# Kernel optimization log

Hardware: AMD Instinct MI355X
Metric: run time of the kernel (lower is better)

The kernel has to match this reference:

```python
import jax, jax.numpy as jnp
import numpy as np

MAX_SEQLEN = 2048  # static max sequence length (flash varlen APIs take this as a host arg)


def setup_inputs() -> dict:
    key = jax.random.key(0)
    k1, k2, k3 = jax.random.split(key, 3)
    T, H, D = 8192, 8, 128
    B = 4
    q = jax.random.normal(k1, (T, H, D), dtype=jnp.float32)
    k = jax.random.normal(k2, (T, H, D), dtype=jnp.float32)
    v = jax.random.normal(k3, (T, H, D), dtype=jnp.float32)
    cu = (jnp.arange(B + 1, dtype=jnp.int32) * (T // B))  # [0,2048,4096,6144,8192]
    return {"q": q, "k": k, "v": v, "cu_seqlens_q": cu, "cu_seqlens_k": cu}


def reference(q, k, v, cu_seqlens_q, cu_seqlens_k):
    """Varlen (ragged) multi-head attention, non-causal (flash_attn varlen default).

    q,k,v: [T, H, D] packed over sequences; cu_seqlens: [B+1] boundaries.
    Gathers each sequence into a padded [B, S, H, D] layout, computes
    per-sequence softmax(q k^T / sqrt(D)) v with padding masked, then
    scatters back to packed [T, H, D].
    """
    T, H, D = q.shape
    B = cu_seqlens_q.shape[0] - 1
    S = MAX_SEQLEN
    scale = 1.0 / jnp.sqrt(jnp.asarray(D, q.dtype))

    pos = jnp.arange(S)
    q_start = cu_seqlens_q[:-1]
    k_start = cu_seqlens_k[:-1]
    q_len = jnp.diff(cu_seqlens_q)  # [B]
    k_len = jnp.diff(cu_seqlens_k)

    q_idx = jnp.clip(q_start[:, None] + pos[None, :], 0, T - 1)  # [B, S]
    k_idx = jnp.clip(k_start[:, None] + pos[None, :], 0, T - 1)
    q_valid = pos[None, :] < q_len[:, None]  # [B, S]
    k_valid = pos[None, :] < k_len[:, None]

    qb = q[q_idx]  # [B, S, H, D]
    kb = k[k_idx]
    vb = v[k_idx]

    scores = jnp.einsum('bqhd,bkhd->bhqk', qb, kb) * scale  # [B, H, S, S]
    neg = jnp.asarray(-1e30, scores.dtype)
    scores = jnp.where(k_valid[:, None, None, :], scores, neg)
    attn = jax.nn.softmax(scores, axis=-1)
    ob = jnp.einsum('bhqk,bkhd->bqhd', attn, vb)  # [B, S, H, D]

    # zero padded query rows, then scatter-add back to packed layout
    ob = jnp.where(q_valid[:, :, None, None], ob, 0.0)
    out = jnp.zeros_like(q).at[q_idx.reshape(-1)].add(ob.reshape(B * S, H, D))
    return out
```

## Files before the change

kernel.cpp:

```cpp
#include <hip/hip_runtime.h>
#include <hip/hip_bf16.h>
#include <stdint.h>

#define HH 8
#define DD 128
#define MAXSEQ 2048
#define QBLK 128
#define KVB 64

typedef float f32x16 __attribute__((ext_vector_type(16)));
typedef short s16x8 __attribute__((ext_vector_type(8)));
typedef uint32_t u32x4v __attribute__((ext_vector_type(4)));

__device__ __forceinline__ unsigned short f2bf(float x) {
  union { float f; uint32_t u; } v; v.f = x;
  uint32_t u = v.u;
  return (unsigned short)((u + 0x7FFFu + ((u >> 16) & 1u)) >> 16);
}

__device__ __forceinline__ void gload_lds16(const unsigned short* g, unsigned short* l) {
  __builtin_amdgcn_global_load_lds((const __attribute__((address_space(1))) void*)g,
                                   (__attribute__((address_space(3))) void*)l, 16, 0, 0);
}

__global__ void kconv(const float* __restrict__ k, unsigned short* __restrict__ kb, int T) {
  long i = (long)blockIdx.x * blockDim.x + threadIdx.x;
  long total = (long)T * HH * DD / 4;
  if (i >= total) return;
  long e = i * 4;
  int d = (int)(e % DD);
  int h = (int)((e / DD) % HH);
  long t = e / (DD * HH);
  float4 a = *(const float4*)(k + e);
  ushort4 o;
  o.x = f2bf(a.x); o.y = f2bf(a.y); o.z = f2bf(a.z); o.w = f2bf(a.w);
  *(ushort4*)(kb + ((size_t)h * T + (size_t)t) * DD + d) = o;
}

__global__ void vtrans(const float* __restrict__ v, unsigned short* __restrict__ vt, int T) {
  __shared__ float tile[64][65];
  const int t0 = blockIdx.x * 64;
  const int d0 = blockIdx.y * 64;
  const int h = blockIdx.z;
  const int tid = threadIdx.x;
  const int row = tid >> 2;
  const int c0 = (tid & 3) * 16;
  const int tr = min(t0 + row, T - 1);
  const float* src = v + ((size_t)tr * HH + h) * DD + d0 + c0;
#pragma unroll
  for (int cc = 0; cc < 16; cc += 4) {
    float4 x = *(const float4*)(src + cc);
    tile[row][c0 + cc + 0] = x.x;
    tile[row][c0 + cc + 1] = x.y;
    tile[row][c0 + cc + 2] = x.z;
    tile[row][c0 + cc + 3] = x.w;
  }
  __syncthreads();
  unsigned short* dst = vt + ((size_t)h * DD + d0 + row) * (size_t)T + t0 + c0;
#pragma unroll
  for (int cc = 0; cc < 16; cc += 4) {
    if (t0 + c0 + cc + 3 < T) {
      ushort4 o;
      o.x = f2bf(tile[c0 + cc + 0][row]);
      o.y = f2bf(tile[c0 + cc + 1][row]);
      o.z = f2bf(tile[c0 + cc + 2][row]);
      o.w = f2bf(tile[c0 + cc + 3][row]);
      *(ushort4*)(dst + cc) = o;
    }
  }
}

__global__ __launch_bounds__(256, 2)
void attn_main(const float* __restrict__ q,
               const unsigned short* __restrict__ kb,
               const unsigned short* __restrict__ vt,
               const int* __restrict__ cuq,
               const int* __restrict__ cuk,
               float* __restrict__ out,
               int T, int BH) {
  extern __shared__ __align__(16) unsigned short smem[];

  const int bid = blockIdx.x;
  const int bh = bid % BH;
  const int qt = bid / BH;
  const int b = bh / HH, h = bh % HH;
  const int qs = cuq[b], qe = cuq[b + 1];
  const int ks = cuk[b], ke = cuk[b + 1];
  const int nq = min(qe - qs, MAXSEQ);
  const int nk = min(ke - ks, MAXSEQ);
  if (qt * QBLK >= nq || nk <= 0) return;

  const int tid = threadIdx.x;
  const int wave = tid >> 6;
  const int lane = tid & 63;
  const int lo = lane & 31;
  const int hi = lane >> 5;
  const int wbase8 = (tid & ~63) * 8;

  const unsigned short* kbh = kb + (size_t)h * T * DD;
  const unsigned short* vth = vt + (size_t)h * DD * (size_t)T;

  const float SC = (1.0f / 11.313708498984761f) * 1.4426950408889634f;
  const int qrow = qt * QBLK + wave * 32 + lo;
  const int qg = qs + min(qrow, nq - 1);
  const float* qp = q + ((size_t)qg * HH + h) * DD;
  s16x8 qf[8];
#pragma unroll
  for (int s = 0; s < 8; ++s) {
    const float* p0 = qp + s * 16 + hi * 8;
    float4 a = *(const float4*)(p0);
    float4 c = *(const float4*)(p0 + 4);
    union { unsigned short us[8]; s16x8 v; } u;
    u.us[0] = f2bf(a.x * SC); u.us[1] = f2bf(a.y * SC);
    u.us[2] = f2bf(a.z * SC); u.us[3] = f2bf(a.w * SC);
    u.us[4] = f2bf(c.x * SC); u.us[5] = f2bf(c.y * SC);
    u.us[6] = f2bf(c.z * SC); u.us[7] = f2bf(c.w * SC);
    qf[s] = u.v;
  }

  f32x16 Oa[4];
#pragma unroll
  for (int i = 0; i < 4; ++i)
#pragma unroll
    for (int r = 0; r < 16; ++r) Oa[i][r] = 0.0f;

  float m_run = -__builtin_inff();
  float l_run = 0.0f;

  const int nkt = (nk + KVB - 1) / KVB;

  auto stage = [&](int buf, int kt) {
    const int k0 = ks + kt * KVB;
    unsigned short* Kb = smem + buf * 8192;
    unsigned short* Vb = smem + 16384 + buf * 8192;
#pragma unroll
    for (int r = 0; r < 4; ++r) {
      const int g = r * 256 + tid;
      const int key = g >> 4, seg = g & 15;
      const int col = (seg * 8) ^ ((key & 7) << 3);
      const int gk = min(k0 + key, T - 1);
      gload_lds16(kbh + (size_t)gk * DD + col, Kb + (size_t)(r * 256) * 8 + wbase8);
    }
#pragma unroll
    for (int r = 0; r < 4; ++r) {
      const int g = r * 256 + tid;
      const int dr = g >> 3, sg = g & 7;
      const int colk = (sg * 8) ^ ((dr & 7) << 3);
      const int tc = min(k0 + colk, T - 8);
      gload_lds16(vth + (size_t)dr * T + tc, Vb + (size_t)(r * 256) * 8 + wbase8);
    }
  };

  stage(0, 0);
  __syncthreads();

  int cur = 0;
  for (int kt = 0; kt < nkt; ++kt) {
    if (kt + 1 < nkt) stage(cur ^ 1, kt + 1);

    const unsigned short* Kb = smem + cur * 8192;
    const unsigned short* Vb = smem + 16384 + cur * 8192;

    f32x16 st0, st1;
#pragma unroll
    for (int r = 0; r < 16; ++r) { st0[r] = 0.0f; st1[r] = 0.0f; }
    __builtin_amdgcn_s_setprio(1);
#pragma unroll
    for (int s = 0; s < 8; ++s) {
      {
        const int key = lo;
        const int idx = (key * DD + s * 16 + hi * 8) ^ ((key & 7) << 3);
        s16x8 kf = *(const s16x8*)(&Kb[idx]);
        st0 = __builtin_amdgcn_mfma_f32_32x32x16_bf16(kf, qf[s], st0, 0, 0, 0);
      }
      {
        const int key = 32 + lo;
        const int idx = (key * DD + s * 16 + hi * 8) ^ ((key & 7) << 3);
        s16x8 kf = *(const s16x8*)(&Kb[idx]);
        st1 = __builtin_amdgcn_mfma_f32_32x32x16_bf16(kf, qf[s], st1, 0, 0, 0);
      }
    }
    __builtin_amdgcn_s_setprio(0);

    if (kt * KVB + KVB > nk) {
#pragma unroll
      for (int r = 0; r < 16; ++r) {
        const int base = (r & 3) + 8 * (r >> 2) + 4 * hi;
        if (kt * KVB + base >= nk) st0[r] = -__builtin_inff();
        if (kt * KVB + 32 + base >= nk) st1[r] = -__builtin_inff();
      }
    }

    float tmax = -__builtin_inff();
#pragma unroll
    for (int r = 0; r < 16; ++r) tmax = fmaxf(tmax, fmaxf(st0[r], st1[r]));
    tmax = fmaxf(tmax, __shfl_xor(tmax, 32));

    if (!__all(tmax <= m_run + 8.0f)) {
      const float m_new = fmaxf(m_run, tmax);
      const float alpha = __builtin_amdgcn_exp2f(m_run - m_new);
      l_run *= alpha;
      m_run = m_new;
#pragma unroll
      for (int r = 0; r < 16; ++r) {
        const int src = (r & 3) + 8 * (r >> 2) + 4 * hi;
        const float af = __shfl(alpha, src);
        Oa[0][r] *= af; Oa[1][r] *= af; Oa[2][r] *= af; Oa[3][r] *= af;
      }
    }

    float p[32];
    float psum = 0.0f;
#pragma unroll
    for (int r = 0; r < 16; ++r) {
      p[r] = __builtin_amdgcn_exp2f(st0[r] - m_run);
      p[16 + r] = __builtin_amdgcn_exp2f(st1[r] - m_run);
      psum += p[r] + p[16 + r];
    }
    psum += __shfl_xor(psum, 32);
    l_run += psum;

    uint32_t ownu[16];
#pragma unroll
    for (int c = 0; c < 8; ++c) {
      const int t = c >> 2, rb = 4 * (c & 3);
      uint32_t w0, w1;
      asm("v_cvt_pk_bf16_f32 %0, %1, %2" : "=v"(w0) : "v"(p[t * 16 + rb + 0]), "v"(p[t * 16 + rb + 1]));
      asm("v_cvt_pk_bf16_f32 %0, %1, %2" : "=v"(w1) : "v"(p[t * 16 + rb + 2]), "v"(p[t * 16 + rb + 3]));
      ownu[c * 2 + 0] = w0;
      ownu[c * 2 + 1] = w1;
    }

    __builtin_amdgcn_s_setprio(1);
#pragma unroll
    for (int ks2 = 0; ks2 < 4; ++ks2) {
      uint32_t a0 = ownu[4 * ks2 + 0], b0 = ownu[4 * ks2 + 2];
      uint32_t a1 = ownu[4 * ks2 + 1], b1 = ownu[4 * ks2 + 3];
      asm("v_permlane32_swap_b32 %0, %1" : "+v"(a0), "+v"(b0));
      asm("v_permlane32_swap_b32 %0, %1" : "+v"(a1), "+v"(b1));
      union { uint32_t u[4]; s16x8 v; } pu;
      pu.u[0] = a0; pu.u[1] = a1; pu.u[2] = b0; pu.u[3] = b1;
#pragma unroll
      for (int dt = 0; dt < 4; ++dt) {
        const int d = dt * 32 + lo;
        const int idx = (d * KVB + ks2 * 16 + hi * 8) ^ ((d & 7) << 3);
        s16x8 vf = *(const s16x8*)(&Vb[idx]);
        Oa[dt] = __builtin_amdgcn_mfma_f32_32x32x16_bf16(pu.v, vf, Oa[dt], 0, 0, 0);
      }
    }
    __builtin_amdgcn_s_setprio(0);

    if (kt + 1 < nkt) {
      __syncthreads();
      cur ^= 1;
    }
  }

  const float linv = 1.0f / l_run;
#pragma unroll
  for (int r = 0; r < 16; ++r) {
    const int src = (r & 3) + 8 * (r >> 2) + 4 * hi;
    const float li = __shfl(linv, src);
    const int qirow = qt * QBLK + wave * 32 + src;
    if (qirow < nq) {
      float* op = out + ((size_t)(qs + qirow) * HH + h) * DD;
      op[0 * 32 + lo] = Oa[0][r] * li;
      op[1 * 32 + lo] = Oa[1][r] * li;
      op[2 * 32 + lo] = Oa[2][r] * li;
      op[3 * 32 + lo] = Oa[3][r] * li;
    }
  }
}

extern "C" void kernel_launch(void* const* d_in, const int* in_sizes, int n_in,
                              void* d_out, int out_size, void* d_ws, size_t ws_size,
                              hipStream_t stream) {
  const float* q = (const float*)d_in[0];
  const float* k = (const float*)d_in[1];
  const float* v = (const float*)d_in[2];
  const int* cuq = (const int*)d_in[3];
  const int* cuk = (const int*)d_in[4];
  float* out = (float*)d_out;
  const int T = in_sizes[0] / (HH * DD);
  const int B = in_sizes[3] - 1;

  hipMemsetAsync(d_out, 0, (size_t)out_size * sizeof(float), stream);

  unsigned short* kb = (unsigned short*)d_ws;
  unsigned short* vt = kb + (size_t)T * HH * DD;
  const size_t need = (size_t)T * HH * DD * 2 * 2;
  if (ws_size < need) return;

  {
    long total4 = (long)T * HH * DD / 4;
    int blocks = (int)((total4 + 255) / 256);
    kconv<<<blocks, 256, 0, stream>>>(k, kb, T);
  }
  {
    dim3 g((unsigned)((T + 63) / 64), DD / 64, HH);
    vtrans<<<g, 256, 0, stream>>>(v, vt, T);
  }
  {
    const int BH = B * HH;
    const int scap = MAXSEQ < T ? MAXSEQ : T;
    const int qtiles = (scap + QBLK - 1) / QBLK;
    attn_main<<<BH * qtiles, 256, 65536, stream>>>(q, kb, vt, cuq, cuk, out, T, BH);
  }
}
```

Measured before the change: 115.5 us.

## Split KV range across two wave groups per block and merge softmax partials

The attention block grows to 512 threads, with two groups of four waves each processing half of the key range (up to 1024 keys each) over 32-key tiles. At the end the two partial softmax states are merged through shared memory. The V tile layout in LDS is reworked for the smaller tile. The full-output memset is replaced by a kernel that zeroes only rows not covered by any sequence. The intent is more waves per CU to hide latency and less memset traffic, at the cost of smaller MFMA tiles per sync, more barriers, and a merge epilogue.

```diff
diff --git a/kernel.cpp b/kernel.cpp
--- a/kernel.cpp
+++ b/kernel.cpp
@@ -6,11 +6,10 @@
 #define DD 128
 #define MAXSEQ 2048
 #define QBLK 128
-#define KVB 64
+#define KVB 32
 
 typedef float f32x16 __attribute__((ext_vector_type(16)));
 typedef short s16x8 __attribute__((ext_vector_type(8)));
-typedef uint32_t u32x4v __attribute__((ext_vector_type(4)));
 
 __device__ __forceinline__ unsigned short f2bf(float x) {
   union { float f; uint32_t u; } v; v.f = x;
@@ -21,6 +20,22 @@
 __device__ __forceinline__ void gload_lds16(const unsigned short* g, unsigned short* l) {
   __builtin_amdgcn_global_load_lds((const __attribute__((address_space(1))) void*)g,
                                    (__attribute__((address_space(3))) void*)l, 16, 0, 0);
+}
+
+__global__ void zero_rows(const int* __restrict__ cuq, float* __restrict__ out, int T, int B) {
+  const int t = blockIdx.x * blockDim.x + threadIdx.x;
+  if (t >= T) return;
+  bool covered = false;
+  for (int b = 0; b < B; ++b) {
+    const int s = cuq[b];
+    const int len = min(cuq[b + 1] - s, MAXSEQ);
+    if (t >= s && t < s + len) covered = true;
+  }
+  if (!covered) {
+    float4* p = (float4*)(out + (size_t)t * HH * DD);
+#pragma unroll 4
+    for (int i = 0; i < HH * DD / 4; ++i) p[i] = float4{0.f, 0.f, 0.f, 0.f};
+  }
 }
 
 __global__ void kconv(const float* __restrict__ k, unsigned short* __restrict__ kb, int T) {
@@ -70,7 +85,7 @@
   }
 }
 
-__global__ __launch_bounds__(256, 2)
+__global__ __launch_bounds__(512, 4)
 void attn_main(const float* __restrict__ q,
                const unsigned short* __restrict__ kb,
                const unsigned short* __restrict__ vt,
@@ -95,13 +110,14 @@
   const int lane = tid & 63;
   const int lo = lane & 31;
   const int hi = lane >> 5;
-  const int wbase8 = (tid & ~63) * 8;
+  const int wq = wave & 3;
+  const int wk = wave >> 2;
 
   const unsigned short* kbh = kb + (size_t)h * T * DD;
   const unsigned short* vth = vt + (size_t)h * DD * (size_t)T;
 
   const float SC = (1.0f / 11.313708498984761f) * 1.4426950408889634f;
-  const int qrow = qt * QBLK + wave * 32 + lo;
+  const int qrow = qt * QBLK + wq * 32 + lo;
   const int qg = qs + min(qrow, nq - 1);
   const float* qp = q + ((size_t)qg * HH + h) * DD;
   s16x8 qf[8];
@@ -127,27 +143,28 @@
   float m_run = -__builtin_inff();
   float l_run = 0.0f;
 
-  const int nkt = (nk + KVB - 1) / KVB;
+  const int len_wk = min(nk - wk * 1024, 1024);
+  const int myT = len_wk > 0 ? (len_wk + KVB - 1) / KVB : 0;
+  const int nkt = (min(nk, 1024) + KVB - 1) / KVB;
 
   auto stage = [&](int buf, int kt) {
-    const int k0 = ks + kt * KVB;
-    unsigned short* Kb = smem + buf * 8192;
-    unsigned short* Vb = smem + 16384 + buf * 8192;
-#pragma unroll
-    for (int r = 0; r < 4; ++r) {
-      const int g = r * 256 + tid;
-      const int key = g >> 4, seg = g & 15;
-      const int col = (seg * 8) ^ ((key & 7) << 3);
-      const int gk = min(k0 + key, T - 1);
-      gload_lds16(kbh + (size_t)gk * DD + col, Kb + (size_t)(r * 256) * 8 + wbase8);
-    }
-#pragma unroll
-    for (int r = 0; r < 4; ++r) {
-      const int g = r * 256 + tid;
-      const int dr = g >> 3, sg = g & 7;
-      const int colk = (sg * 8) ^ ((dr & 7) << 3);
-      const int tc = min(k0 + colk, T - 8);
-      gload_lds16(vth + (size_t)dr * T + tc, Vb + (size_t)(r * 256) * 8 + wbase8);
+#pragma unroll
+    for (int wkk = 0; wkk < 2; ++wkk) {
+      unsigned short* slot = smem + (size_t)(wkk * 2 + buf) * 8192;
+      const int kb0 = ks + wkk * 1024 + kt * KVB;
+      {
+        const int key = tid >> 4, seg = tid & 15;
+        const int col = (seg * 8) ^ ((key & 7) << 3);
+        const int gk = min(kb0 + key, T - 1);
+        gload_lds16(kbh + (size_t)gk * DD + col, slot + (size_t)(tid & ~63) * 8);
+      }
+      {
+        const int r = tid >> 3, ph = tid & 7;
+        const int tt = ph ^ (r & 7);
+        const int d = 2 * r + (tt >> 2);
+        const int tc = min(kb0 + (tt & 3) * 8, T - 8);
+        gload_lds16(vth + (size_t)d * T + tc, slot + 4096 + (size_t)(tid & ~63) * 8);
+      }
     }
   };
 
@@ -158,97 +175,89 @@
   for (int kt = 0; kt < nkt; ++kt) {
     if (kt + 1 < nkt) stage(cur ^ 1, kt + 1);
 
-    const unsigned short* Kb = smem + cur * 8192;
-    const unsigned short* Vb = smem + 16384 + cur * 8192;
-
-    f32x16 st0, st1;
-#pragma unroll
-    for (int r = 0; r < 16; ++r) { st0[r] = 0.0f; st1[r] = 0.0f; }
-    __builtin_amdgcn_s_setprio(1);
-#pragma unroll
-    for (int s = 0; s < 8; ++s) {
-      {
-        const int key = lo;
-        const int idx = (key * DD + s * 16 + hi * 8) ^ ((key & 7) << 3);
-        s16x8 kf = *(const s16x8*)(&Kb[idx]);
-        st0 = __builtin_amdgcn_mfma_f32_32x32x16_bf16(kf, qf[s], st0, 0, 0, 0);
-      }
-      {
-        const int key = 32 + lo;
-        const int idx = (key * DD + s * 16 + hi * 8) ^ ((key & 7) << 3);
-        s16x8 kf = *(const s16x8*)(&Kb[idx]);
-        st1 = __builtin_amdgcn_mfma_f32_32x32x16_bf16(kf, qf[s], st1, 0, 0, 0);
-      }
-    }
-    __builtin_amdgcn_s_setprio(0);
-
-    if (kt * KVB + KVB > nk) {
+    if (kt < myT) {
+      const unsigned short* Kl = smem + (size_t)(wk * 2 + cur) * 8192;
+      const unsigned short* Vl = Kl + 4096;
+
+      f32x16 st;
+#pragma unroll
+      for (int r = 0; r < 16; ++r) st[r] = 0.0f;
+      __builtin_amdgcn_s_setprio(1);
+#pragma unroll
+      for (int s = 0; s < 8; ++s) {
+        const int idx = (lo * DD + s * 16 + hi * 8) ^ ((lo & 7) << 3);
+        s16x8 kf = *(const s16x8*)(&Kl[idx]);
+        st = __builtin_amdgcn_mfma_f32_32x32x16_bf16(kf, qf[s], st, 0, 0, 0);
+      }
+      __builtin_amdgcn_s_setprio(0);
+
+      const int lim = len_wk - kt * KVB;
+      if (lim < KVB) {
+#pragma unroll
+        for (int r = 0; r < 16; ++r) {
+          const int base = (r & 3) + 8 * (r >> 2) + 4 * hi;
+          if (base >= lim) st[r] = -__builtin_inff();
+        }
+      }
+
+      float tmax = -__builtin_inff();
+#pragma unroll
+      for (int r = 0; r < 16; ++r) tmax = fmaxf(tmax, st[r]);
+      tmax = fmaxf(tmax, __shfl_xor(tmax, 32));
+
+      if (!__all(tmax <= m_run + 8.0f)) {
+        const float m_new = fmaxf(m_run, tmax);
+        const float alpha = __builtin_amdgcn_exp2f(m_run - m_new);
+        l_run *= alpha;
+        m_run = m_new;
+#pragma unroll
+        for (int r = 0; r < 16; ++r) {
+          const int src = (r & 3) + 8 * (r >> 2) + 4 * hi;
+          const float af = __shfl(alpha, src);
+          Oa[0][r] *= af; Oa[1][r] *= af; Oa[2][r] *= af; Oa[3][r] *= af;
+        }
+      }
+
+      float p[16];
+      float psum = 0.0f;
 #pragma unroll
       for (int r = 0; r < 16; ++r) {
-        const int base = (r & 3) + 8 * (r >> 2) + 4 * hi;
-        if (kt * KVB + base >= nk) st0[r] = -__builtin_inff();
-        if (kt * KVB + 32 + base >= nk) st1[r] = -__builtin_inff();
-      }
-    }
-
-    float tmax = -__builtin_inff();
-#pragma unroll
-    for (int r = 0; r < 16; ++r) tmax = fmaxf(tmax, fmaxf(st0[r], st1[r]));
-    tmax = fmaxf(tmax, __shfl_xor(tmax, 32));
-
-    if (!__all(tmax <= m_run + 8.0f)) {
-      const float m_new = fmaxf(m_run, tmax);
-      const float alpha = __builtin_amdgcn_exp2f(m_run - m_new);
-      l_run *= alpha;
-      m_run = m_new;
-#pragma unroll
-      for (int r = 0; r < 16; ++r) {
-        const int src = (r & 3) + 8 * (r >> 2) + 4 * hi;
-        const float af = __shfl(alpha, src);
-        Oa[0][r] *= af; Oa[1][r] *= af; Oa[2][r] *= af; Oa[3][r] *= af;
-      }
-    }
-
-    float p[32];
-    float psum = 0.0f;
-#pragma unroll
-    for (int r = 0; r < 16; ++r) {
-      p[r] = __builtin_amdgcn_exp2f(st0[r] - m_run);
-      p[16 + r] = __builtin_amdgcn_exp2f(st1[r] - m_run);
-      psum += p[r] + p[16 + r];
-    }
-    psum += __shfl_xor(psum, 32);
-    l_run += psum;
-
-    uint32_t ownu[16];
-#pragma unroll
-    for (int c = 0; c < 8; ++c) {
-      const int t = c >> 2, rb = 4 * (c & 3);
-      uint32_t w0, w1;
-      asm("v_cvt_pk_bf16_f32 %0, %1, %2" : "=v"(w0) : "v"(p[t * 16 + rb + 0]), "v"(p[t * 16 + rb + 1]));
-      asm("v_cvt_pk_bf16_f32 %0, %1, %2" : "=v"(w1) : "v"(p[t * 16 + rb + 2]), "v"(p[t * 16 + rb + 3]));
-      ownu[c * 2 + 0] = w0;
-      ownu[c * 2 + 1] = w1;
-    }
-
-    __builtin_amdgcn_s_setprio(1);
-#pragma unroll
-    for (int ks2 = 0; ks2 < 4; ++ks2) {
-      uint32_t a0 = ownu[4 * ks2 + 0], b0 = ownu[4 * ks2 + 2];
-      uint32_t a1 = ownu[4 * ks2 + 1], b1 = ownu[4 * ks2 + 3];
-      asm("v_permlane32_swap_b32 %0, %1" : "+v"(a0), "+v"(b0));
-      asm("v_permlane32_swap_b32 %0, %1" : "+v"(a1), "+v"(b1));
-      union { uint32_t u[4]; s16x8 v; } pu;
-      pu.u[0] = a0; pu.u[1] = a1; pu.u[2] = b0; pu.u[3] = b1;
-#pragma unroll
-      for (int dt = 0; dt < 4; ++dt) {
-        const int d = dt * 32 + lo;
-        const int idx = (d * KVB + ks2 * 16 + hi * 8) ^ ((d & 7) << 3);
-        s16x8 vf = *(const s16x8*)(&Vb[idx]);
-        Oa[dt] = __builtin_amdgcn_mfma_f32_32x32x16_bf16(pu.v, vf, Oa[dt], 0, 0, 0);
-      }
-    }
-    __builtin_amdgcn_s_setprio(0);
+        p[r] = __builtin_amdgcn_exp2f(st[r] - m_run);
+        psum += p[r];
+      }
+      psum += __shfl_xor(psum, 32);
+      l_run += psum;
+
+      uint32_t ownu[8];
+#pragma unroll
+      for (int c = 0; c < 4; ++c) {
+        uint32_t w0, w1;
+        asm("v_cvt_pk_bf16_f32 %0, %1, %2" : "=v"(w0) : "v"(p[4 * c + 0]), "v"(p[4 * c + 1]));
+        asm("v_cvt_pk_bf16_f32 %0, %1, %2" : "=v"(w1) : "v"(p[4 * c + 2]), "v"(p[4 * c + 3]));
+        ownu[c * 2 + 0] = w0;
+        ownu[c * 2 + 1] = w1;
+      }
+
+      __builtin_amdgcn_s_setprio(1);
+#pragma unroll
+      for (int ks2 = 0; ks2 < 2; ++ks2) {
+        uint32_t a0 = ownu[4 * ks2 + 0], b0 = ownu[4 * ks2 + 2];
+        uint32_t a1 = ownu[4 * ks2 + 1], b1 = ownu[4 * ks2 + 3];
+        asm("v_permlane32_swap_b32 %0, %1" : "+v"(a0), "+v"(b0));
+        asm("v_permlane32_swap_b32 %0, %1" : "+v"(a1), "+v"(b1));
+        union { uint32_t u[4]; s16x8 v; } pu;
+        pu.u[0] = a0; pu.u[1] = a1; pu.u[2] = b0; pu.u[3] = b1;
+#pragma unroll
+        for (int dt = 0; dt < 4; ++dt) {
+          const int r = dt * 16 + (lo >> 1);
+          const int ph = ((lo & 1) * 4 + ks2 * 2 + hi) ^ ((lo >> 1) & 7);
+          const int idx = r * 64 + ph * 8;
+          s16x8 vf = *(const s16x8*)(&Vl[idx]);
+          Oa[dt] = __builtin_amdgcn_mfma_f32_32x32x16_bf16(pu.v, vf, Oa[dt], 0, 0, 0);
+        }
+      }
+      __builtin_amdgcn_s_setprio(0);
+    }
 
     if (kt + 1 < nkt) {
       __syncthreads();
@@ -256,18 +265,51 @@
     }
   }
 
-  const float linv = 1.0f / l_run;
-#pragma unroll
-  for (int r = 0; r < 16; ++r) {
-    const int src = (r & 3) + 8 * (r >> 2) + 4 * hi;
-    const float li = __shfl(linv, src);
-    const int qirow = qt * QBLK + wave * 32 + src;
-    if (qirow < nq) {
-      float* op = out + ((size_t)(qs + qirow) * HH + h) * DD;
-      op[0 * 32 + lo] = Oa[0][r] * li;
-      op[1 * 32 + lo] = Oa[1][r] * li;
-      op[2 * 32 + lo] = Oa[2][r] * li;
-      op[3 * 32 + lo] = Oa[3][r] * li;
+  float* fsm = (float*)smem;
+  __syncthreads();
+  if (hi == 0) {
+    fsm[wk * 256 + wq * 64 + lo] = m_run;
+    fsm[wk * 256 + wq * 64 + 32 + lo] = l_run;
+  }
+  __syncthreads();
+  const int po = (wk ^ 1) * 256 + wq * 64 + lo;
+  const float m_o = fsm[po];
+  const float l_o = fsm[po + 32];
+  const float mstar = fmaxf(m_run, m_o);
+  const float a_own = (l_run == 0.f) ? 0.f : __builtin_amdgcn_exp2f(m_run - mstar);
+  const float a_oth = (l_o == 0.f) ? 0.f : __builtin_amdgcn_exp2f(m_o - mstar);
+  __syncthreads();
+
+  if (wk == 1) {
+#pragma unroll
+    for (int r = 0; r < 16; ++r) {
+      const int src = (r & 3) + 8 * (r >> 2) + 4 * hi;
+      const float af = __shfl(a_own, src);
+      float* row = fsm + (size_t)wq * 4096 + (size_t)src * 128;
+      row[0 * 32 + lo] = Oa[0][r] * af;
+      row[1 * 32 + lo] = Oa[1][r] * af;
+      row[2 * 32 + lo] = Oa[2][r] * af;
+      row[3 * 32 + lo] = Oa[3][r] * af;
+    }
+  }
+  __syncthreads();
+  if (wk == 0) {
+    const float lst = a_own * l_run + a_oth * l_o;
+    const float linv = 1.0f / lst;
+#pragma unroll
+    for (int r = 0; r < 16; ++r) {
+      const int src = (r & 3) + 8 * (r >> 2) + 4 * hi;
+      const float af = __shfl(a_own, src);
+      const float li = __shfl(linv, src);
+      const int qirow = qt * QBLK + wq * 32 + src;
+      if (qirow < nq) {
+        const float* row = fsm + (size_t)wq * 4096 + (size_t)src * 128;
+        float* op = out + ((size_t)(qs + qirow) * HH + h) * DD;
+        op[0 * 32 + lo] = (Oa[0][r] * af + row[0 * 32 + lo]) * li;
+        op[1 * 32 + lo] = (Oa[1][r] * af + row[1 * 32 + lo]) * li;
+        op[2 * 32 + lo] = (Oa[2][r] * af + row[2 * 32 + lo]) * li;
+        op[3 * 32 + lo] = (Oa[3][r] * af + row[3 * 32 + lo]) * li;
+      }
     }
   }
 }
@@ -284,14 +326,15 @@
   const int T = in_sizes[0] / (HH * DD);
   const int B = in_sizes[3] - 1;
 
-  hipMemsetAsync(d_out, 0, (size_t)out_size * sizeof(float), stream);
-
   unsigned short* kb = (unsigned short*)d_ws;
   unsigned short* vt = kb + (size_t)T * HH * DD;
   const size_t need = (size_t)T * HH * DD * 2 * 2;
   if (ws_size < need) return;
 
   {
+    zero_rows<<<(T + 255) / 256, 256, 0, stream>>>(cuq, out, T, B);
+  }
+  {
     long total4 = (long)T * HH * DD / 4;
     int blocks = (int)((total4 + 255) / 256);
     kconv<<<blocks, 256, 0, stream>>>(k, kb, T);
@@ -304,6 +347,6 @@
     const int BH = B * HH;
     const int scap = MAXSEQ < T ? MAXSEQ : T;
     const int qtiles = (scap + QBLK - 1) / QBLK;
-    attn_main<<<BH * qtiles, 256, 65536, stream>>>(q, kb, vt, cuq, cuk, out, T, BH);
-  }
-}
+    attn_main<<<BH * qtiles, 512, 65536, stream>>>(q, kb, vt, cuq, cuk, out, T, BH);
+  }
+}
```

Result: slower. 183.2 us (+58.5%).

## Prefetch K/V LDS fragments into registers and zero only uncovered output rows

Applied to the files above, without the earlier changes.

Reads all K fragments from LDS into registers before issuing the next tile's async global-to-LDS staging. V fragments are loaded in two halves, interleaved with the softmax work, so LDS latency overlaps compute instead of sitting inline with each MFMA. It also replaces the full-output memset with a small kernel that zeroes only token rows not covered by any sequence, cutting redundant output writes. The register prefetch raises VGPR pressure, which could reduce occupancy or cause spills.

```diff
diff --git a/kernel.cpp b/kernel.cpp
--- a/kernel.cpp
+++ b/kernel.cpp
@@ -10,7 +10,6 @@
 
 typedef float f32x16 __attribute__((ext_vector_type(16)));
 typedef short s16x8 __attribute__((ext_vector_type(8)));
-typedef uint32_t u32x4v __attribute__((ext_vector_type(4)));
 
 __device__ __forceinline__ unsigned short f2bf(float x) {
   union { float f; uint32_t u; } v; v.f = x;
@@ -21,6 +20,22 @@
 __device__ __forceinline__ void gload_lds16(const unsigned short* g, unsigned short* l) {
   __builtin_amdgcn_global_load_lds((const __attribute__((address_space(1))) void*)g,
                                    (__attribute__((address_space(3))) void*)l, 16, 0, 0);
+}
+
+__global__ void zero_rows(const int* __restrict__ cuq, float* __restrict__ out, int T, int B) {
+  const int t = blockIdx.x * blockDim.x + threadIdx.x;
+  if (t >= T) return;
+  bool covered = false;
+  for (int b = 0; b < B; ++b) {
+    const int s = cuq[b];
+    const int len = min(cuq[b + 1] - s, MAXSEQ);
+    if (t >= s && t < s + len) covered = true;
+  }
+  if (!covered) {
+    float4* p = (float4*)(out + (size_t)t * HH * DD);
+#pragma unroll 4
+    for (int i = 0; i < HH * DD / 4; ++i) p[i] = float4{0.f, 0.f, 0.f, 0.f};
+  }
 }
 
 __global__ void kconv(const float* __restrict__ k, unsigned short* __restrict__ kb, int T) {
@@ -131,15 +146,15 @@
 
   auto stage = [&](int buf, int kt) {
     const int k0 = ks + kt * KVB;
-    unsigned short* Kb = smem + buf * 8192;
-    unsigned short* Vb = smem + 16384 + buf * 8192;
+    unsigned short* Kd = smem + buf * 8192;
+    unsigned short* Vd = smem + 16384 + buf * 8192;
 #pragma unroll
     for (int r = 0; r < 4; ++r) {
       const int g = r * 256 + tid;
       const int key = g >> 4, seg = g & 15;
       const int col = (seg * 8) ^ ((key & 7) << 3);
       const int gk = min(k0 + key, T - 1);
-      gload_lds16(kbh + (size_t)gk * DD + col, Kb + (size_t)(r * 256) * 8 + wbase8);
+      gload_lds16(kbh + (size_t)gk * DD + col, Kd + (size_t)(r * 256) * 8 + wbase8);
     }
 #pragma unroll
     for (int r = 0; r < 4; ++r) {
@@ -147,7 +162,7 @@
       const int dr = g >> 3, sg = g & 7;
       const int colk = (sg * 8) ^ ((dr & 7) << 3);
       const int tc = min(k0 + colk, T - 8);
-      gload_lds16(vth + (size_t)dr * T + tc, Vb + (size_t)(r * 256) * 8 + wbase8);
+      gload_lds16(vth + (size_t)dr * T + tc, Vd + (size_t)(r * 256) * 8 + wbase8);
     }
   };
 
@@ -156,31 +171,40 @@
 
   int cur = 0;
   for (int kt = 0; kt < nkt; ++kt) {
-    if (kt + 1 < nkt) stage(cur ^ 1, kt + 1);
-
     const unsigned short* Kb = smem + cur * 8192;
     const unsigned short* Vb = smem + 16384 + cur * 8192;
 
+    s16x8 kf[16];
+#pragma unroll
+    for (int s = 0; s < 8; ++s) {
+      const int i0 = (lo * DD + s * 16 + hi * 8) ^ ((lo & 7) << 3);
+      const int i1 = ((32 + lo) * DD + s * 16 + hi * 8) ^ ((lo & 7) << 3);
+      kf[2 * s] = *(const s16x8*)(&Kb[i0]);
+      kf[2 * s + 1] = *(const s16x8*)(&Kb[i1]);
+    }
+
+    if (kt + 1 < nkt) stage(cur ^ 1, kt + 1);
+
     f32x16 st0, st1;
 #pragma unroll
     for (int r = 0; r < 16; ++r) { st0[r] = 0.0f; st1[r] = 0.0f; }
     __builtin_amdgcn_s_setprio(1);
 #pragma unroll
     for (int s = 0; s < 8; ++s) {
-      {
-        const int key = lo;
-        const int idx = (key * DD + s * 16 + hi * 8) ^ ((key & 7) << 3);
-        s16x8 kf = *(const s16x8*)(&Kb[idx]);
-        st0 = __builtin_amdgcn_mfma_f32_32x32x16_bf16(kf, qf[s], st0, 0, 0, 0);
-      }
-      {
-        const int key = 32 + lo;
-        const int idx = (key * DD + s * 16 + hi * 8) ^ ((key & 7) << 3);
-        s16x8 kf = *(const s16x8*)(&Kb[idx]);
-        st1 = __builtin_amdgcn_mfma_f32_32x32x16_bf16(kf, qf[s], st1, 0, 0, 0);
-      }
+      st0 = __builtin_amdgcn_mfma_f32_32x32x16_bf16(kf[2 * s], qf[s], st0, 0, 0, 0);
+      st1 = __builtin_amdgcn_mfma_f32_32x32x16_bf16(kf[2 * s + 1], qf[s], st1, 0, 0, 0);
     }
     __builtin_amdgcn_s_setprio(0);
+
+    s16x8 vfA[8];
+#pragma unroll
+    for (int ks2 = 0; ks2 < 2; ++ks2)
+#pragma unroll
+      for (int dt = 0; dt < 4; ++dt) {
+        const int d = dt * 32 + lo;
+        const int idx = (d * KVB + ks2 * 16 + hi * 8) ^ ((d & 7) << 3);
+        vfA[ks2 * 4 + dt] = *(const s16x8*)(&Vb[idx]);
+      }
 
     if (kt * KVB + KVB > nk) {
 #pragma unroll
@@ -231,6 +255,16 @@
       ownu[c * 2 + 1] = w1;
     }
 
+    s16x8 vfB[8];
+#pragma unroll
+    for (int ks2 = 0; ks2 < 2; ++ks2)
+#pragma unroll
+      for (int dt = 0; dt < 4; ++dt) {
+        const int d = dt * 32 + lo;
+        const int idx = (d * KVB + (ks2 + 2) * 16 + hi * 8) ^ ((d & 7) << 3);
+        vfB[ks2 * 4 + dt] = *(const s16x8*)(&Vb[idx]);
+      }
+
     __builtin_amdgcn_s_setprio(1);
 #pragma unroll
     for (int ks2 = 0; ks2 < 4; ++ks2) {
@@ -242,9 +276,7 @@
       pu.u[0] = a0; pu.u[1] = a1; pu.u[2] = b0; pu.u[3] = b1;
 #pragma unroll
       for (int dt = 0; dt < 4; ++dt) {
-        const int d = dt * 32 + lo;
-        const int idx = (d * KVB + ks2 * 16 + hi * 8) ^ ((d & 7) << 3);
-        s16x8 vf = *(const s16x8*)(&Vb[idx]);
+        s16x8 vf = (ks2 < 2) ? vfA[ks2 * 4 + dt] : vfB[(ks2 - 2) * 4 + dt];
         Oa[dt] = __builtin_amdgcn_mfma_f32_32x32x16_bf16(pu.v, vf, Oa[dt], 0, 0, 0);
       }
     }
@@ -284,13 +316,14 @@
   const int T = in_sizes[0] / (HH * DD);
   const int B = in_sizes[3] - 1;
 
-  hipMemsetAsync(d_out, 0, (size_t)out_size * sizeof(float), stream);
-
   unsigned short* kb = (unsigned short*)d_ws;
   unsigned short* vt = kb + (size_t)T * HH * DD;
   const size_t need = (size_t)T * HH * DD * 2 * 2;
   if (ws_size < need) return;
 
+  {
+    zero_rows<<<(T + 255) / 256, 256, 0, stream>>>(cuq, out, T, B);
+  }
   {
     long total4 = (long)T * HH * DD / 4;
     int blocks = (int)((total4 + 255) / 256);
```

Result: no change. 114.1 us (-1.3%).

## Load K fragments directly from pre-swizzled global layout, halve KV tile

Applied to the files above, without the earlier changes.

K is pre-converted into an MFMA-fragment-ordered layout so each lane loads its K operands straight into registers from global memory, bypassing LDS. Only V is staged through a smaller double-buffered LDS tile, and the KV block drops from 64 to 32 keys, with the loop unrolled into a two-buffer ping-pong. The full output memset is replaced by a kernel that zeros only rows not covered by any sequence. This lowers LDS footprint and traffic, at the cost of more global loads per block, more iterations with softmax and barrier overhead, and an added kernel launch.

```diff
diff --git a/kernel.cpp b/kernel.cpp
--- a/kernel.cpp
+++ b/kernel.cpp
@@ -6,11 +6,10 @@
 #define DD 128
 #define MAXSEQ 2048
 #define QBLK 128
-#define KVB 64
+#define KVB 32
 
 typedef float f32x16 __attribute__((ext_vector_type(16)));
 typedef short s16x8 __attribute__((ext_vector_type(8)));
-typedef uint32_t u32x4v __attribute__((ext_vector_type(4)));
 
 __device__ __forceinline__ unsigned short f2bf(float x) {
   union { float f; uint32_t u; } v; v.f = x;
@@ -23,18 +22,42 @@
                                    (__attribute__((address_space(3))) void*)l, 16, 0, 0);
 }
 
-__global__ void kconv(const float* __restrict__ k, unsigned short* __restrict__ kb, int T) {
-  long i = (long)blockIdx.x * blockDim.x + threadIdx.x;
-  long total = (long)T * HH * DD / 4;
-  if (i >= total) return;
-  long e = i * 4;
-  int d = (int)(e % DD);
-  int h = (int)((e / DD) % HH);
-  long t = e / (DD * HH);
-  float4 a = *(const float4*)(k + e);
-  ushort4 o;
-  o.x = f2bf(a.x); o.y = f2bf(a.y); o.z = f2bf(a.z); o.w = f2bf(a.w);
-  *(ushort4*)(kb + ((size_t)h * T + (size_t)t) * DD + d) = o;
+__global__ void zero_rows(const int* __restrict__ cuq, float* __restrict__ out, int T, int B) {
+  const int t = blockIdx.x * blockDim.x + threadIdx.x;
+  if (t >= T) return;
+  bool covered = false;
+  for (int b = 0; b < B; ++b) {
+    const int s = cuq[b];
+    const int len = min(cuq[b + 1] - s, MAXSEQ);
+    if (t >= s && t < s + len) covered = true;
+  }
+  if (!covered) {
+    float4* p = (float4*)(out + (size_t)t * HH * DD);
+#pragma unroll 4
+    for (int i = 0; i < HH * DD / 4; ++i) p[i] = float4{0.f, 0.f, 0.f, 0.f};
+  }
+}
+
+__global__ void kconv2(const float* __restrict__ k, unsigned short* __restrict__ kb2, int T) {
+  const int TBc = T >> 5;
+  const int total = TBc * HH * 512;
+  const int u = blockIdx.x * blockDim.x + threadIdx.x;
+  if (u >= total) return;
+  const int lp = u & 63;
+  const int key = lp & 31, hi = lp >> 5;
+  int r = u >> 6;
+  const int s = r & 7; r >>= 3;
+  const int tb = r % TBc;
+  const int h = r / TBc;
+  const int t = tb * 32 + key;
+  const int d = s * 16 + hi * 8;
+  const float* src = k + ((size_t)t * HH + h) * DD + d;
+  float4 a = *(const float4*)src;
+  float4 c = *(const float4*)(src + 4);
+  union { unsigned short us[8]; uint4 q; } w;
+  w.us[0] = f2bf(a.x); w.us[1] = f2bf(a.y); w.us[2] = f2bf(a.z); w.us[3] = f2bf(a.w);
+  w.us[4] = f2bf(c.x); w.us[5] = f2bf(c.y); w.us[6] = f2bf(c.z); w.us[7] = f2bf(c.w);
+  *(uint4*)(kb2 + (size_t)u * 8) = w.q;
 }
 
 __global__ void vtrans(const float* __restrict__ v, unsigned short* __restrict__ vt, int T) {
@@ -72,14 +95,15 @@
 
 __global__ __launch_bounds__(256, 2)
 void attn_main(const float* __restrict__ q,
-               const unsigned short* __restrict__ kb,
+               const unsigned short* __restrict__ kb2,
                const unsigned short* __restrict__ vt,
                const int* __restrict__ cuq,
                const int* __restrict__ cuk,
                float* __restrict__ out,
                int T, int BH) {
-  extern __shared__ __align__(16) unsigned short smem[];
-
+  __shared__ __align__(16) unsigned short Vl[2][4096];
+
+  const int TBc = T >> 5;
   const int bid = blockIdx.x;
   const int bh = bid % BH;
   const int qt = bid / BH;
@@ -97,7 +121,8 @@
   const int hi = lane >> 5;
   const int wbase8 = (tid & ~63) * 8;
 
-  const unsigned short* kbh = kb + (size_t)h * T * DD;
+  const int kb32 = ks >> 5;
+  const unsigned short* kb2h = kb2 + (size_t)h * TBc * 4096;
   const unsigned short* vth = vt + (size_t)h * DD * (size_t)T;
 
   const float SC = (1.0f / 11.313708498984761f) * 1.4426950408889634f;
@@ -129,71 +154,47 @@
 
   const int nkt = (nk + KVB - 1) / KVB;
 
-  auto stage = [&](int buf, int kt) {
+  auto loadK = [&](s16x8(&kf)[8], int kt) {
+    const size_t base = (size_t)min(kb32 + kt, TBc - 1) * 4096;
+#pragma unroll
+    for (int s = 0; s < 8; ++s)
+      kf[s] = *(const s16x8*)(kb2h + base + s * 512 + lane * 8);
+  };
+
+  auto stageV = [&](int buf, int kt) {
     const int k0 = ks + kt * KVB;
-    unsigned short* Kb = smem + buf * 8192;
-    unsigned short* Vb = smem + 16384 + buf * 8192;
-#pragma unroll
-    for (int r = 0; r < 4; ++r) {
-      const int g = r * 256 + tid;
-      const int key = g >> 4, seg = g & 15;
-      const int col = (seg * 8) ^ ((key & 7) << 3);
-      const int gk = min(k0 + key, T - 1);
-      gload_lds16(kbh + (size_t)gk * DD + col, Kb + (size_t)(r * 256) * 8 + wbase8);
-    }
-#pragma unroll
-    for (int r = 0; r < 4; ++r) {
-      const int g = r * 256 + tid;
-      const int dr = g >> 3, sg = g & 7;
-      const int colk = (sg * 8) ^ ((dr & 7) << 3);
-      const int tc = min(k0 + colk, T - 8);
-      gload_lds16(vth + (size_t)dr * T + tc, Vb + (size_t)(r * 256) * 8 + wbase8);
+#pragma unroll
+    for (int r = 0; r < 2; ++r) {
+      const int u = r * 256 + tid;
+      const int d = u >> 2, slot = u & 3;
+      const int c = slot ^ ((d >> 1) & 3);
+      const int tc = min(k0 + c * 8, T - 8);
+      gload_lds16(vth + (size_t)d * T + tc, &Vl[buf][r * 2048 + wbase8]);
     }
   };
 
-  stage(0, 0);
-  __syncthreads();
-
-  int cur = 0;
-  for (int kt = 0; kt < nkt; ++kt) {
-    if (kt + 1 < nkt) stage(cur ^ 1, kt + 1);
-
-    const unsigned short* Kb = smem + cur * 8192;
-    const unsigned short* Vb = smem + 16384 + cur * 8192;
-
-    f32x16 st0, st1;
-#pragma unroll
-    for (int r = 0; r < 16; ++r) { st0[r] = 0.0f; st1[r] = 0.0f; }
+  auto body = [&](const s16x8(&kf)[8], int buf, int kt) {
+    f32x16 st;
+#pragma unroll
+    for (int r = 0; r < 16; ++r) st[r] = 0.0f;
     __builtin_amdgcn_s_setprio(1);
 #pragma unroll
-    for (int s = 0; s < 8; ++s) {
-      {
-        const int key = lo;
-        const int idx = (key * DD + s * 16 + hi * 8) ^ ((key & 7) << 3);
-        s16x8 kf = *(const s16x8*)(&Kb[idx]);
-        st0 = __builtin_amdgcn_mfma_f32_32x32x16_bf16(kf, qf[s], st0, 0, 0, 0);
-      }
-      {
-        const int key = 32 + lo;
-        const int idx = (key * DD + s * 16 + hi * 8) ^ ((key & 7) << 3);
-        s16x8 kf = *(const s16x8*)(&Kb[idx]);
-        st1 = __builtin_amdgcn_mfma_f32_32x32x16_bf16(kf, qf[s], st1, 0, 0, 0);
-      }
-    }
+    for (int s = 0; s < 8; ++s)
+      st = __builtin_amdgcn_mfma_f32_32x32x16_bf16(kf[s], qf[s], st, 0, 0, 0);
     __builtin_amdgcn_s_setprio(0);
 
-    if (kt * KVB + KVB > nk) {
+    const int lim = nk - kt * KVB;
+    if (lim < KVB) {
 #pragma unroll
       for (int r = 0; r < 16; ++r) {
         const int base = (r & 3) + 8 * (r >> 2) + 4 * hi;
-        if (kt * KVB + base >= nk) st0[r] = -__builtin_inff();
-        if (kt * KVB + 32 + base >= nk) st1[r] = -__builtin_inff();
+        if (base >= lim) st[r] = -__builtin_inff();
       }
     }
 
     float tmax = -__builtin_inff();
 #pragma unroll
-    for (int r = 0; r < 16; ++r) tmax = fmaxf(tmax, fmaxf(st0[r], st1[r]));
+    for (int r = 0; r < 16; ++r) tmax = fmaxf(tmax, st[r]);
     tmax = fmaxf(tmax, __shfl_xor(tmax, 32));
 
     if (!__all(tmax <= m_run + 8.0f)) {
@@ -209,31 +210,29 @@
       }
     }
 
-    float p[32];
+    float p[16];
     float psum = 0.0f;
 #pragma unroll
     for (int r = 0; r < 16; ++r) {
-      p[r] = __builtin_amdgcn_exp2f(st0[r] - m_run);
-      p[16 + r] = __builtin_amdgcn_exp2f(st1[r] - m_run);
-      psum += p[r] + p[16 + r];
+      p[r] = __builtin_amdgcn_exp2f(st[r] - m_run);
+      psum += p[r];
     }
     psum += __shfl_xor(psum, 32);
     l_run += psum;
 
-    uint32_t ownu[16];
-#pragma unroll
-    for (int c = 0; c < 8; ++c) {
-      const int t = c >> 2, rb = 4 * (c & 3);
+    uint32_t ownu[8];
+#pragma unroll
+    for (int c = 0; c < 4; ++c) {
       uint32_t w0, w1;
-      asm("v_cvt_pk_bf16_f32 %0, %1, %2" : "=v"(w0) : "v"(p[t * 16 + rb + 0]), "v"(p[t * 16 + rb + 1]));
-      asm("v_cvt_pk_bf16_f32 %0, %1, %2" : "=v"(w1) : "v"(p[t * 16 + rb + 2]), "v"(p[t * 16 + rb + 3]));
+      asm("v_cvt_pk_bf16_f32 %0, %1, %2" : "=v"(w0) : "v"(p[4 * c + 0]), "v"(p[4 * c + 1]));
+      asm("v_cvt_pk_bf16_f32 %0, %1, %2" : "=v"(w1) : "v"(p[4 * c + 2]), "v"(p[4 * c + 3]));
       ownu[c * 2 + 0] = w0;
       ownu[c * 2 + 1] = w1;
     }
 
     __builtin_amdgcn_s_setprio(1);
 #pragma unroll
-    for (int ks2 = 0; ks2 < 4; ++ks2) {
+    for (int ks2 = 0; ks2 < 2; ++ks2) {
       uint32_t a0 = ownu[4 * ks2 + 0], b0 = ownu[4 * ks2 + 2];
       uint32_t a1 = ownu[4 * ks2 + 1], b1 = ownu[4 * ks2 + 3];
       asm("v_permlane32_swap_b32 %0, %1" : "+v"(a0), "+v"(b0));
@@ -242,17 +241,28 @@
       pu.u[0] = a0; pu.u[1] = a1; pu.u[2] = b0; pu.u[3] = b1;
 #pragma unroll
       for (int dt = 0; dt < 4; ++dt) {
-        const int d = dt * 32 + lo;
-        const int idx = (d * KVB + ks2 * 16 + hi * 8) ^ ((d & 7) << 3);
-        s16x8 vf = *(const s16x8*)(&Vb[idx]);
+        const int slot = (ks2 * 2 + hi) ^ ((lo >> 1) & 3);
+        const int idx = (dt * 32 + lo) * 32 + slot * 8;
+        s16x8 vf = *(const s16x8*)(&Vl[buf][idx]);
         Oa[dt] = __builtin_amdgcn_mfma_f32_32x32x16_bf16(pu.v, vf, Oa[dt], 0, 0, 0);
       }
     }
     __builtin_amdgcn_s_setprio(0);
-
+  };
+
+  s16x8 kfA[8], kfB[8];
+  loadK(kfA, 0);
+  stageV(0, 0);
+  __syncthreads();
+
+  for (int kt = 0; kt < nkt; kt += 2) {
+    if (kt + 1 < nkt) { loadK(kfB, kt + 1); stageV(1, kt + 1); }
+    body(kfA, 0, kt);
+    __syncthreads();
     if (kt + 1 < nkt) {
+      if (kt + 2 < nkt) { loadK(kfA, kt + 2); stageV(0, kt + 2); }
+      body(kfB, 1, kt + 1);
       __syncthreads();
-      cur ^= 1;
     }
   }
 
@@ -284,17 +294,17 @@
   const int T = in_sizes[0] / (HH * DD);
   const int B = in_sizes[3] - 1;
 
-  hipMemsetAsync(d_out, 0, (size_t)out_size * sizeof(float), stream);
-
-  unsigned short* kb = (unsigned short*)d_ws;
-  unsigned short* vt = kb + (size_t)T * HH * DD;
+  unsigned short* kb2 = (unsigned short*)d_ws;
+  unsigned short* vt = kb2 + (size_t)T * HH * DD;
   const size_t need = (size_t)T * HH * DD * 2 * 2;
   if (ws_size < need) return;
 
   {
-    long total4 = (long)T * HH * DD / 4;
-    int blocks = (int)((total4 + 255) / 256);
-    kconv<<<blocks, 256, 0, stream>>>(k, kb, T);
+    zero_rows<<<(T + 255) / 256, 256, 0, stream>>>(cuq, out, T, B);
+  }
+  {
+    const int total = (T >> 5) * HH * 512;
+    kconv2<<<(total + 255) / 256, 256, 0, stream>>>(k, kb2, T);
   }
   {
     dim3 g((unsigned)((T + 63) / 64), DD / 64, HH);
@@ -304,6 +314,6 @@
     const int BH = B * HH;
     const int scap = MAXSEQ < T ? MAXSEQ : T;
     const int qtiles = (scap + QBLK - 1) / QBLK;
-    attn_main<<<BH * qtiles, 256, 65536, stream>>>(q, kb, vt, cuq, cuk, out, T, BH);
-  }
-}
+    attn_main<<<BH * qtiles, 256, 0, stream>>>(q, kb2, vt, cuq, cuk, out, T, BH);
+  }
+}
```

Result: slower. 119.8 us (+3.7%).
